# Kernel tuning notes

Hardware: AMD Instinct MI355X
Metric: run time of the kernel (lower is better)

Reference implementation:

```python
import jax, jax.numpy as jnp
import numpy as np
import math

B, S, D, H = 2, 2048, 768, 12
HD = D // H


def setup_inputs() -> dict:
    key = jax.random.key(0)
    ks = jax.random.split(key, 9)
    scale = 1.0 / math.sqrt(D)
    x = jax.random.normal(ks[0], (B, S, D), dtype=jnp.float32)
    # causal mask: True where attention is allowed (query i attends to key j<=i)
    mask = jnp.tril(jnp.ones((S, S), dtype=bool))[None, None]  # [1,1,S,S]
    wq = jax.random.normal(ks[1], (D, D), dtype=jnp.float32) * scale
    bq = jnp.zeros((D,), dtype=jnp.float32)
    wk = jax.random.normal(ks[2], (D, D), dtype=jnp.float32) * scale
    bk = jnp.zeros((D,), dtype=jnp.float32)
    wv = jax.random.normal(ks[3], (D, D), dtype=jnp.float32) * scale
    bv = jnp.zeros((D,), dtype=jnp.float32)
    wo = jax.random.normal(ks[4], (D, D), dtype=jnp.float32) * scale
    bo = jnp.zeros((D,), dtype=jnp.float32)
    return {"x": x, "mask": mask, "wq": wq, "bq": bq, "wk": wk, "bk": bk,
            "wv": wv, "bv": bv, "wo": wo, "bo": bo}


def reference(x, mask, wq, bq, wk, bk, wv, bv, wo, bo):
    b, s, d = x.shape
    # projections (flax Linear: y = x @ kernel + bias)
    q = (x @ wq + bq).reshape(b, s, H, HD).transpose(0, 2, 1, 3)  # [b,h,s,hd]
    k = (x @ wk + bk).reshape(b, s, H, HD).transpose(0, 2, 1, 3)
    v = (x @ wv + bv).reshape(b, s, H, HD).transpose(0, 2, 1, 3)
    scores = jnp.einsum('bhqd,bhkd->bhqk', q, k) / math.sqrt(HD)  # [b,h,s,s]
    scores = jnp.where(mask, scores, -jnp.inf)
    attn = jax.nn.softmax(scores, axis=-1)
    out = jnp.einsum('bhqk,bhkd->bhqd', attn, v)  # [b,h,s,hd]
    out = out.transpose(0, 2, 1, 3).reshape(b, s, d)
    return out @ wo + bo
```

## Files before the change

### kernel.cpp

```cpp
#include <hip/hip_runtime.h>
#include <math.h>

#define BATCH 2
#define SEQ   2048
#define DMODEL 768
#define NHEAD 12
#define HDIM  64

typedef unsigned short u16;
typedef __attribute__((ext_vector_type(8))) short bf16x8;
typedef __attribute__((ext_vector_type(4))) float f32x4;
typedef __attribute__((ext_vector_type(8))) unsigned short us8;
typedef __attribute__((ext_vector_type(4))) unsigned short us4;

__device__ __forceinline__ u16 f2bf(float f) {
    union { float f; unsigned u; } v; v.f = f;
    unsigned u = v.u;
    u += 0x7fff + ((u >> 16) & 1);
    return (u16)(u >> 16);
}

__device__ __forceinline__ u16 f2bf_trunc(float f) {
    union { float f; unsigned u; } v; v.f = f;
    return (u16)(v.u >> 16);
}

__device__ __forceinline__ void g2l16(const void* g, void* l) {
    __builtin_amdgcn_global_load_lds(
        (const __attribute__((address_space(1))) unsigned int*)g,
        (__attribute__((address_space(3))) unsigned int*)(unsigned int)(unsigned long long)(uintptr_t)l,
        16, 0, 0);
}

__device__ __forceinline__ void stage_rows(const u16* g, u16* lds, int nrows,
                                           int tid) {
    const int row = tid >> 2, col = (tid & 3) * 8;
    g2l16(g + (size_t)row * DMODEL + col, lds + tid * 8);
    if (nrows == 128) {
        g2l16(g + (size_t)(row + 64) * DMODEL + col, lds + 2048 + tid * 8);
    } else if (nrows == 96) {
        if (tid < 128)
            g2l16(g + (size_t)(row + 64) * DMODEL + col, lds + 2048 + tid * 8);
    }
}

__global__ __launch_bounds__(256) void prep(const float* __restrict__ x,
                                            const float* __restrict__ w0,
                                            const float* __restrict__ w1,
                                            const float* __restrict__ w2,
                                            const float* __restrict__ w3,
                                            u16* __restrict__ xb,
                                            u16* __restrict__ Wt_all) {
    __shared__ float t[32][33];
    const int bid = blockIdx.x;
    if (bid < 3072) {
        int i = bid * 256 + threadIdx.x;
        float4 v = ((const float4*)x)[i];
        us4 o;
        o.x = f2bf(v.x); o.y = f2bf(v.y); o.z = f2bf(v.z); o.w = f2bf(v.w);
        *(us4*)&xb[(size_t)i * 4] = o;
    } else {
        const int wid = bid - 3072;
        const int z  = wid / 576;
        const int rr = wid % 576;
        const int by = rr / 24, bx = rr % 24;
        const float* W = z == 0 ? w0 : z == 1 ? w1 : z == 2 ? w2 : w3;
        u16* Wt = Wt_all + (size_t)z * DMODEL * DMODEL;

        int tx = threadIdx.x & 31, ty = threadIdx.x >> 5;
        int xg = bx * 32 + tx;
        #pragma unroll
        for (int j = 0; j < 32; j += 8)
            t[ty + j][tx] = W[(size_t)(by * 32 + ty + j) * DMODEL + xg];
        __syncthreads();
        int x2 = by * 32 + tx;
        #pragma unroll
        for (int j = 0; j < 32; j += 8)
            Wt[(size_t)(bx * 32 + ty + j) * DMODEL + x2] = f2bf(t[tx][ty + j]);
    }
}

__global__ __launch_bounds__(256) void gemm_qkv(
    const u16* __restrict__ xb, const u16* __restrict__ WtQK,
    const u16* __restrict__ WtV,
    const float* __restrict__ bq, const float* __restrict__ bk,
    const float* __restrict__ bv,
    u16* __restrict__ QK, u16* __restrict__ Vt) {

    __shared__ __align__(16) u16 As[128 * 32];
    __shared__ __align__(16) u16 Bs[128 * 32];

    const int tid  = threadIdx.x;
    const int lane = tid & 63;
    const int w    = tid >> 6;
    const int quad = lane >> 4, l16 = lane & 15;
    const int wm   = w >> 1, wn = w & 1;
    const int b    = blockIdx.x;

    if (b < 512) {
        const int m0 = (b >> 4) * 128;
        const int n0 = (b & 15) * 96;
        f32x4 acc[4][3] = {};
        for (int k0 = 0; k0 < DMODEL; k0 += 32) {
            stage_rows(xb   + (size_t)m0 * DMODEL + k0, As, 128, tid);
            stage_rows(WtQK + (size_t)n0 * DMODEL + k0, Bs,  96, tid);
            __syncthreads();
            bf16x8 af[4], bfr[3];
            #pragma unroll
            for (int i = 0; i < 4; ++i)
                af[i] = *(const bf16x8*)&As[(wm * 64 + i * 16 + l16) * 32 + quad * 8];
            #pragma unroll
            for (int j = 0; j < 3; ++j)
                bfr[j] = *(const bf16x8*)&Bs[(wn * 48 + j * 16 + l16) * 32 + quad * 8];
            #pragma unroll
            for (int i = 0; i < 4; ++i)
                #pragma unroll
                for (int j = 0; j < 3; ++j)
                    acc[i][j] = __builtin_amdgcn_mfma_f32_16x16x32_bf16(af[i], bfr[j], acc[i][j], 0, 0, 0);
            __syncthreads();
        }
        const size_t n_elem = (size_t)BATCH * SEQ * DMODEL;
        #pragma unroll
        for (int j = 0; j < 3; ++j) {
            const int n     = n0 + wn * 48 + j * 16 + l16;
            const int which = n / 768;
            const int nn    = n - which * 768;
            const float bias  = (which == 0 ? bq : bk)[nn];
            const float scale = (which == 0) ? 0.125f : 1.0f;
            const int h = nn >> 6, hd = nn & 63;
            u16* outw = QK + (size_t)which * n_elem;
            #pragma unroll
            for (int i = 0; i < 4; ++i) {
                const int mbase = m0 + wm * 64 + i * 16 + quad * 4;
                #pragma unroll
                for (int r = 0; r < 4; ++r) {
                    const int m  = mbase + r;
                    const int b_ = m >> 11, s_ = m & 2047;
                    outw[(size_t)((b_ * NHEAD + h) * SEQ + s_) * HDIM + hd] =
                        f2bf((acc[i][j][r] + bias) * scale);
                }
            }
        }
    } else {
        const int vj = b - 512;
        const int m0 = (vj & 7) * 96;
        const int n0 = (vj >> 3) * 128;
        f32x4 acc[3][4] = {};
        for (int k0 = 0; k0 < DMODEL; k0 += 32) {
            stage_rows(WtV + (size_t)m0 * DMODEL + k0, As,  96, tid);
            stage_rows(xb  + (size_t)n0 * DMODEL + k0, Bs, 128, tid);
            __syncthreads();
            bf16x8 af[3], bfr[4];
            #pragma unroll
            for (int i = 0; i < 3; ++i)
                af[i] = *(const bf16x8*)&As[(wm * 48 + i * 16 + l16) * 32 + quad * 8];
            #pragma unroll
            for (int j = 0; j < 4; ++j)
                bfr[j] = *(const bf16x8*)&Bs[(wn * 64 + j * 16 + l16) * 32 + quad * 8];
            #pragma unroll
            for (int i = 0; i < 3; ++i)
                #pragma unroll
                for (int j = 0; j < 4; ++j)
                    acc[i][j] = __builtin_amdgcn_mfma_f32_16x16x32_bf16(af[i], bfr[j], acc[i][j], 0, 0, 0);
            __syncthreads();
        }
        #pragma unroll
        for (int i = 0; i < 3; ++i) {
            const int rbase = m0 + wm * 48 + i * 16 + quad * 4;
            #pragma unroll
            for (int r = 0; r < 4; ++r) {
                const int row_g = rbase + r;
                const float bias = bv[row_g];
                const int h = row_g >> 6, hd = row_g & 63;
                #pragma unroll
                for (int j = 0; j < 4; ++j) {
                    const int col_g = n0 + wn * 64 + j * 16 + l16;
                    const int b_ = col_g >> 11, s_ = col_g & 2047;
                    Vt[(size_t)((b_ * NHEAD + h) * HDIM + hd) * SEQ + s_] =
                        f2bf(acc[i][j][r] + bias);
                }
            }
        }
    }
}

__global__ __launch_bounds__(256) void gemm_out(
    const u16* __restrict__ Ag, const u16* __restrict__ Bt,
    const float* __restrict__ bo, float* __restrict__ out) {

    __shared__ __align__(16) u16 As[64 * 32];
    __shared__ __align__(16) u16 Bs[64 * 32];

    const int tid  = threadIdx.x;
    const int lane = tid & 63;
    const int w    = tid >> 6;
    const int quad = lane >> 4, l16 = lane & 15;
    const int wm   = w >> 1, wn = w & 1;
    const int m0 = blockIdx.x * 64, n0 = blockIdx.y * 64;

    const int rowA = tid >> 2;
    const int kch  = (tid & 3) * 8;

    f32x4 acc[2][2] = {};

    for (int k0 = 0; k0 < DMODEL; k0 += 32) {
        g2l16(Ag + (size_t)(m0 + rowA) * DMODEL + k0 + kch, As + tid * 8);
        g2l16(Bt + (size_t)(n0 + rowA) * DMODEL + k0 + kch, Bs + tid * 8);
        __syncthreads();

        bf16x8 af[2], bfr[2];
        #pragma unroll
        for (int i = 0; i < 2; ++i)
            af[i] = *(const bf16x8*)&As[(wm * 32 + i * 16 + l16) * 32 + quad * 8];
        #pragma unroll
        for (int j = 0; j < 2; ++j)
            bfr[j] = *(const bf16x8*)&Bs[(wn * 32 + j * 16 + l16) * 32 + quad * 8];
        #pragma unroll
        for (int i = 0; i < 2; ++i)
            #pragma unroll
            for (int j = 0; j < 2; ++j)
                acc[i][j] = __builtin_amdgcn_mfma_f32_16x16x32_bf16(af[i], bfr[j], acc[i][j], 0, 0, 0);
        __syncthreads();
    }

    #pragma unroll
    for (int i = 0; i < 2; ++i) {
        const int mbase = m0 + wm * 32 + i * 16 + quad * 4;
        #pragma unroll
        for (int r = 0; r < 4; ++r) {
            const int m = mbase + r;
            #pragma unroll
            for (int j = 0; j < 2; ++j) {
                const int n = n0 + wn * 32 + j * 16 + l16;
                out[(size_t)m * DMODEL + n] = acc[i][j][r] + bo[n];
            }
        }
    }
}

__global__ __launch_bounds__(256) void flash_attn_mfma(
    const u16* __restrict__ Q, const u16* __restrict__ K,
    const u16* __restrict__ Vt, u16* __restrict__ A) {

    __shared__ __align__(16) u16 Kl[64 * 72];
    __shared__ __align__(16) u16 Vl[64 * 72];
    __shared__ __align__(16) u16 Pl[4][16 * 72];

    const int tid  = threadIdx.x;
    const int lane = tid & 63;
    const int w    = tid >> 6;
    const int quad = lane >> 4;
    const int l16  = lane & 15;

    const int bh = blockIdx.x;
    const int p  = blockIdx.y;
    const int uq = (w < 2) ? p : 63 - p;
    const int wrow0 = uq * 32 + (w & 1) * 16;
    const int wlast = wrow0 + 15;

    const size_t base = (size_t)bh * SEQ * HDIM;
    const u16* Qg = Q + base;
    const u16* Kg = K + base;
    const u16* Vg = Vt + base;

    bf16x8 qf0 = *(const bf16x8*)&Qg[(size_t)(wrow0 + l16) * 64 + quad * 8];
    bf16x8 qf1 = *(const bf16x8*)&Qg[(size_t)(wrow0 + l16) * 64 + quad * 8 + 32];

    f32x4 o[4] = {};
    float l_acc[4] = {0.f, 0.f, 0.f, 0.f};

    const int qrow = wrow0 + quad * 4;
    const int uB = 63 - p;
    const int tc = (32 * uB + 31) / 64 + 1;

    const int pwbase = 2 * quad + (l16 >> 3);
    const int prd0   = (quad + 2 * (l16 >> 2)) & 7;
    u16* Pw = Pl[w];
    const u16* pr0 = &Pw[l16 * 72 + prd0 * 8];
    const u16* pr1 = &Pw[l16 * 72 + (prd0 ^ 4) * 8];

    for (int t2 = 0; t2 < tc; ++t2) {
        const int j0 = t2 * 64;
        __syncthreads();

        #pragma unroll
        for (int r = 0; r < 2; ++r) {
            int e = tid + r * 256;
            int row = e >> 3, col = (e & 7) * 8;
            *(us8*)&Kl[row * 72 + col] = *(const us8*)&Kg[(size_t)(j0 + row) * 64 + col];
        }
        #pragma unroll
        for (int r = 0; r < 2; ++r) {
            int e = tid + r * 256;
            int d = e >> 3, kc = (e & 7) * 8;
            *(us8*)&Vl[d * 72 + kc] = *(const us8*)&Vg[(size_t)d * SEQ + j0 + kc];
        }
        __syncthreads();

        if (j0 > wlast) continue;

        f32x4 s[4];
        #pragma unroll
        for (int c4 = 0; c4 < 4; ++c4) {
            bf16x8 kf0 = *(const bf16x8*)&Kl[(c4 * 16 + l16) * 72 + quad * 8];
            bf16x8 kf1 = *(const bf16x8*)&Kl[(c4 * 16 + l16) * 72 + quad * 8 + 32];
            f32x4 a2 = {};
            a2 = __builtin_amdgcn_mfma_f32_16x16x32_bf16(qf0, kf0, a2, 0, 0, 0);
            a2 = __builtin_amdgcn_mfma_f32_16x16x32_bf16(qf1, kf1, a2, 0, 0, 0);
            s[c4] = a2;
        }

        if (j0 + 63 > wrow0) {
            #pragma unroll
            for (int c4 = 0; c4 < 4; ++c4) {
                int jg = j0 + c4 * 16 + l16;
                #pragma unroll
                for (int r = 0; r < 4; ++r)
                    if (jg > qrow + r) s[c4][r] = -INFINITY;
            }
        }

        #pragma unroll
        for (int c4 = 0; c4 < 4; ++c4)
            #pragma unroll
            for (int r = 0; r < 4; ++r)
                s[c4][r] = __expf(s[c4][r]);
        #pragma unroll
        for (int r = 0; r < 4; ++r)
            l_acc[r] += (s[0][r] + s[1][r]) + (s[2][r] + s[3][r]);

        #pragma unroll
        for (int c4 = 0; c4 < 4; ++c4) {
            const int pc = ((2 * c4 + pwbase) & 7) * 8 + (l16 & 7);
            #pragma unroll
            for (int r = 0; r < 4; ++r)
                Pw[(quad * 4 + r) * 72 + pc] = f2bf_trunc(s[c4][r]);
        }
        bf16x8 pf0 = *(const bf16x8*)pr0;
        bf16x8 pf1 = *(const bf16x8*)pr1;

        #pragma unroll
        for (int c2 = 0; c2 < 4; ++c2) {
            bf16x8 vf0 = *(const bf16x8*)&Vl[(c2 * 16 + l16) * 72 + quad * 8];
            bf16x8 vf1 = *(const bf16x8*)&Vl[(c2 * 16 + l16) * 72 + quad * 8 + 32];
            o[c2] = __builtin_amdgcn_mfma_f32_16x16x32_bf16(pf0, vf0, o[c2], 0, 0, 0);
            o[c2] = __builtin_amdgcn_mfma_f32_16x16x32_bf16(pf1, vf1, o[c2], 0, 0, 0);
        }
    }

    #pragma unroll
    for (int off = 1; off < 16; off <<= 1)
        #pragma unroll
        for (int r = 0; r < 4; ++r)
            l_acc[r] += __shfl_xor(l_acc[r], off);

    const int b = bh / NHEAD, h = bh % NHEAD;
    #pragma unroll
    for (int r = 0; r < 4; ++r) {
        float inv = 1.0f / l_acc[r];
        int sg = qrow + r;
        u16* dst = A + ((size_t)(b * SEQ + sg)) * DMODEL + h * HDIM;
        #pragma unroll
        for (int c2 = 0; c2 < 4; ++c2)
            dst[c2 * 16 + l16] = f2bf(o[c2][r] * inv);
    }
}

extern "C" void kernel_launch(void* const* d_in, const int* in_sizes, int n_in,
                              void* d_out, int out_size, void* d_ws, size_t ws_size,
                              hipStream_t stream) {
    const float* x  = (const float*)d_in[0];
    const float* wq = (const float*)d_in[2];
    const float* bq = (const float*)d_in[3];
    const float* wk = (const float*)d_in[4];
    const float* bk = (const float*)d_in[5];
    const float* wv = (const float*)d_in[6];
    const float* bv = (const float*)d_in[7];
    const float* wo = (const float*)d_in[8];
    const float* bo = (const float*)d_in[9];
    float* out = (float*)d_out;

    const size_t n_elem = (size_t)BATCH * SEQ * DMODEL;
    const size_t w_elem = (size_t)DMODEL * DMODEL;

    u16* xb     = (u16*)d_ws;
    u16* Wt_all = xb + n_elem;
    u16* Qw     = Wt_all + 4 * w_elem;
    u16* Vtw    = Qw + 2 * n_elem;
    u16* Aw     = Vtw + n_elem;

    dim3 blk(256);

    prep<<<dim3(3072 + 2304), blk, 0, stream>>>(x, wq, wk, wv, wo, xb, Wt_all);

    gemm_qkv<<<dim3(768), blk, 0, stream>>>(xb, Wt_all, Wt_all + 2 * w_elem,
                                            bq, bk, bv, Qw, Vtw);

    flash_attn_mfma<<<dim3(24, 32), blk, 0, stream>>>(Qw, Qw + n_elem, Vtw, Aw);

    gemm_out<<<dim3(64, 12), blk, 0, stream>>>(Aw, Wt_all + 3 * w_elem, bo, out);
}
```

Before: 168.9 us.

## Double-buffer K/V tiles with direct global-to-LDS loads and reorder attention blocks

```diff
diff --git a/kernel.cpp b/kernel.cpp
--- a/kernel.cpp
+++ b/kernel.cpp
@@ -242,8 +242,8 @@
     const u16* __restrict__ Q, const u16* __restrict__ K,
     const u16* __restrict__ Vt, u16* __restrict__ A) {
 
-    __shared__ __align__(16) u16 Kl[64 * 72];
-    __shared__ __align__(16) u16 Vl[64 * 72];
+    __shared__ __align__(16) u16 Kl[2][64 * 64];
+    __shared__ __align__(16) u16 Vl[2][64 * 64];
     __shared__ __align__(16) u16 Pl[4][16 * 72];
 
     const int tid  = threadIdx.x;
@@ -252,26 +252,26 @@
     const int quad = lane >> 4;
     const int l16  = lane & 15;
 
-    const int bh = blockIdx.x;
-    const int p  = blockIdx.y;
-    const int uq = (w < 2) ? p : 63 - p;
-    const int wrow0 = uq * 32 + (w & 1) * 16;
-    const int wlast = wrow0 + 15;
+    const int lin = blockIdx.x;
+    const int cc_ = lin & 255, rk = lin >> 8;
+    const int sid = (rk << 8) + ((rk & 1) ? (255 - cc_) : cc_);
+    const int j   = sid / 24;
+    const int bh  = sid - j * 24;
+    const int tc  = j + 1;
 
     const size_t base = (size_t)bh * SEQ * HDIM;
     const u16* Qg = Q + base;
     const u16* Kg = K + base;
     const u16* Vg = Vt + base;
 
+    const int wrow0 = j * 64 + w * 16;
+    const int qrow  = wrow0 + quad * 4;
+
     bf16x8 qf0 = *(const bf16x8*)&Qg[(size_t)(wrow0 + l16) * 64 + quad * 8];
     bf16x8 qf1 = *(const bf16x8*)&Qg[(size_t)(wrow0 + l16) * 64 + quad * 8 + 32];
 
     f32x4 o[4] = {};
     float l_acc[4] = {0.f, 0.f, 0.f, 0.f};
-
-    const int qrow = wrow0 + quad * 4;
-    const int uB = 63 - p;
-    const int tc = (32 * uB + 31) / 64 + 1;
 
     const int pwbase = 2 * quad + (l16 >> 3);
     const int prd0   = (quad + 2 * (l16 >> 2)) & 7;
@@ -279,41 +279,46 @@
     const u16* pr0 = &Pw[l16 * 72 + prd0 * 8];
     const u16* pr1 = &Pw[l16 * 72 + (prd0 ^ 4) * 8];
 
-    for (int t2 = 0; t2 < tc; ++t2) {
-        const int j0 = t2 * 64;
-        __syncthreads();
-
-        #pragma unroll
-        for (int r = 0; r < 2; ++r) {
-            int e = tid + r * 256;
-            int row = e >> 3, col = (e & 7) * 8;
-            *(us8*)&Kl[row * 72 + col] = *(const us8*)&Kg[(size_t)(j0 + row) * 64 + col];
-        }
-        #pragma unroll
-        for (int r = 0; r < 2; ++r) {
-            int e = tid + r * 256;
-            int d = e >> 3, kc = (e & 7) * 8;
-            *(us8*)&Vl[d * 72 + kc] = *(const us8*)&Vg[(size_t)d * SEQ + j0 + kc];
-        }
-        __syncthreads();
-
-        if (j0 > wlast) continue;
+    auto STAGE = [&](int t, int b) {
+        const int j0 = t * 64;
+        #pragma unroll
+        for (int h = 0; h < 2; ++h) {
+            const int ch = tid + h * 256;
+            const int r  = ch >> 3;
+            const int lc = (ch & 7) ^ (r & 7);
+            g2l16(Kg + (size_t)(j0 + r) * 64 + lc * 8, &Kl[b][ch * 8]);
+            g2l16(Vg + (size_t)r * SEQ + j0 + lc * 8,  &Vl[b][ch * 8]);
+        }
+    };
+
+    STAGE(0, 0);
+    __syncthreads();
+
+    int cur = 0;
+    for (int t = 0; t < tc; ++t) {
+        if (t + 1 < tc) STAGE(t + 1, cur ^ 1);
+
+        const int j0 = t * 64;
+        const u16* Kc = Kl[cur];
+        const u16* Vc = Vl[cur];
 
         f32x4 s[4];
         #pragma unroll
         for (int c4 = 0; c4 < 4; ++c4) {
-            bf16x8 kf0 = *(const bf16x8*)&Kl[(c4 * 16 + l16) * 72 + quad * 8];
-            bf16x8 kf1 = *(const bf16x8*)&Kl[(c4 * 16 + l16) * 72 + quad * 8 + 32];
+            const int krow = c4 * 16 + l16;
+            const int pc = (quad ^ (krow & 7)) * 8;
+            bf16x8 kf0 = *(const bf16x8*)&Kc[krow * 64 + pc];
+            bf16x8 kf1 = *(const bf16x8*)&Kc[krow * 64 + (pc ^ 32)];
             f32x4 a2 = {};
             a2 = __builtin_amdgcn_mfma_f32_16x16x32_bf16(qf0, kf0, a2, 0, 0, 0);
             a2 = __builtin_amdgcn_mfma_f32_16x16x32_bf16(qf1, kf1, a2, 0, 0, 0);
             s[c4] = a2;
         }
 
-        if (j0 + 63 > wrow0) {
+        if (t == tc - 1) {
             #pragma unroll
             for (int c4 = 0; c4 < 4; ++c4) {
-                int jg = j0 + c4 * 16 + l16;
+                const int jg = j0 + c4 * 16 + l16;
                 #pragma unroll
                 for (int r = 0; r < 4; ++r)
                     if (jg > qrow + r) s[c4][r] = -INFINITY;
@@ -341,11 +346,16 @@
 
         #pragma unroll
         for (int c2 = 0; c2 < 4; ++c2) {
-            bf16x8 vf0 = *(const bf16x8*)&Vl[(c2 * 16 + l16) * 72 + quad * 8];
-            bf16x8 vf1 = *(const bf16x8*)&Vl[(c2 * 16 + l16) * 72 + quad * 8 + 32];
+            const int vrow = c2 * 16 + l16;
+            const int vc = (quad ^ (vrow & 7)) * 8;
+            bf16x8 vf0 = *(const bf16x8*)&Vc[vrow * 64 + vc];
+            bf16x8 vf1 = *(const bf16x8*)&Vc[vrow * 64 + (vc ^ 32)];
             o[c2] = __builtin_amdgcn_mfma_f32_16x16x32_bf16(pf0, vf0, o[c2], 0, 0, 0);
             o[c2] = __builtin_amdgcn_mfma_f32_16x16x32_bf16(pf1, vf1, o[c2], 0, 0, 0);
         }
+
+        __syncthreads();
+        cur ^= 1;
     }
 
     #pragma unroll
@@ -396,7 +406,7 @@
     gemm_qkv<<<dim3(768), blk, 0, stream>>>(xb, Wt_all, Wt_all + 2 * w_elem,
                                             bq, bk, bv, Qw, Vtw);
 
-    flash_attn_mfma<<<dim3(24, 32), blk, 0, stream>>>(Qw, Qw + n_elem, Vtw, Aw);
+    flash_attn_mfma<<<dim3(768), blk, 0, stream>>>(Qw, Qw + n_elem, Vtw, Aw);
 
     gemm_out<<<dim3(64, 12), blk, 0, stream>>>(Aw, Wt_all + 3 * w_elem, bo, out);
 }
```

Result: no change. 166.8 us (-1.3%).
